# Kernel optimization log

Measured on AMD Instinct MI355X. Metric: run time of the kernel, lower is better.

The kernel has to match this reference:

```python
import jax, jax.numpy as jnp
import numpy as np

N = 40000      # nodes
E = 640000     # edges
IN_DIM = 128
HID = 128
HEADS = 4
DHEAD = HID // HEADS  # 32
LAYERS = 3
TIMESTEPS = 2
NEG_SLOPE = 0.2


def setup_inputs() -> dict:
    key = jax.random.key(0)
    ks = jax.random.split(key, 16)
    s = 0.05
    inp = {
        "node_feats": jax.random.normal(ks[0], (N, IN_DIM), jnp.float32),
        "src": jax.random.randint(ks[1], (E,), 0, N, jnp.int32),
        "dst": jax.random.randint(ks[2], (E,), 0, N, jnp.int32),
        "proj_W": jax.random.normal(ks[3], (IN_DIM, HID), jnp.float32) * s,
        "proj_b": jnp.zeros((HID,), jnp.float32),
        "fc_W": jax.random.normal(ks[4], (LAYERS, HID, HID), jnp.float32) * s,
        "attn_l": jax.random.normal(ks[5], (LAYERS, HEADS, DHEAD), jnp.float32) * s,
        "attn_r": jax.random.normal(ks[6], (LAYERS, HEADS, DHEAD), jnp.float32) * s,
        "conv_bias": jnp.zeros((LAYERS, HID), jnp.float32),
        "gru_Wih": jax.random.normal(ks[7], (3 * HID, HID), jnp.float32) * s,
        "gru_Whh": jax.random.normal(ks[8], (3 * HID, HID), jnp.float32) * s,
        "gru_bih": jnp.zeros((3 * HID,), jnp.float32),
        "gru_bhh": jnp.zeros((3 * HID,), jnp.float32),
    }
    return inp


def _gat_layer(h, src, dst, fc_W, attn_l, attn_r, bias):
    # h: (N, HID). DGL GATConv: fc -> edge attn -> segment softmax -> scatter sum
    feat = (h @ fc_W).reshape(N, HEADS, DHEAD)
    el = jnp.einsum('nhd,hd->nh', feat, attn_l)  # (N, H)
    er = jnp.einsum('nhd,hd->nh', feat, attn_r)
    e = jax.nn.leaky_relu(el[src] + er[dst], NEG_SLOPE)  # (E, H)
    # segment softmax over incoming edges per destination node
    emax = jax.ops.segment_max(e, dst, num_segments=N)  # (N, H)
    ee = jnp.exp(e - emax[dst])
    denom = jax.ops.segment_sum(ee, dst, num_segments=N)
    alpha = ee / denom[dst]  # (E, H)
    msg = feat[src] * alpha[:, :, None]  # (E, H, D)
    rst = jax.ops.segment_sum(msg, dst, num_segments=N)  # (N, H, D)
    rst = rst + h.reshape(N, HEADS, DHEAD)          # identity residual
    rst = rst + bias.reshape(HEADS, DHEAD)          # learned bias
    return jax.nn.elu(rst).reshape(N, HID)


def _gru_step(x, Wih, Whh, bih, bhh):
    # seq_len == 1, h0 == 0 -> recurrent matmul Whh @ h0 vanishes; b_hh remains
    gi = x @ Wih.T + bih  # (N, 3*HID)
    r = jax.nn.sigmoid(gi[:, :HID] + bhh[:HID])
    z = jax.nn.sigmoid(gi[:, HID:2 * HID] + bhh[HID:2 * HID])
    n = jnp.tanh(gi[:, 2 * HID:] + r * bhh[2 * HID:])
    return (1.0 - z) * n


def reference(node_feats, src, dst, proj_W, proj_b, fc_W, attn_l, attn_r,
              conv_bias, gru_Wih, gru_Whh, gru_bih, gru_bhh):
    h = node_feats @ proj_W + proj_b
    for l in range(LAYERS):
        h = _gat_layer(h, src, dst, fc_W[l], attn_l[l], attn_r[l], conv_bias[l])
    for _ in range(TIMESTEPS):
        h = _gru_step(h, gru_Wih, gru_Whh, gru_bih, gru_bhh)
    return h
```

## Files before the change

kernel.cpp:

```cpp
#include <hip/hip_runtime.h>
#include <hip/hip_bf16.h>

#define NNODES 40000
#define NEDGES 640000
#define M2PAD  40064
#define HID    128
#define PADCAP 920064

typedef __attribute__((ext_vector_type(8))) short bf16x8;
typedef __attribute__((ext_vector_type(4))) float f32x4;

__device__ __forceinline__ float bl(unsigned u){ return __uint_as_float(u << 16); }
__device__ __forceinline__ float bh(unsigned u){ return __uint_as_float(u & 0xFFFF0000u); }
__device__ __forceinline__ unsigned short f2b(float f){
    unsigned u = __float_as_uint(f);
    u = (u + 0x7FFFu + ((u >> 16) & 1u)) >> 16;
    return (unsigned short)u;
}
__device__ __forceinline__ float fast_rcp(float x){ return __builtin_amdgcn_rcpf(x); }

__device__ __forceinline__ void g2l16(const void* g, void* l){
    __builtin_amdgcn_global_load_lds(
        (const __attribute__((address_space(1))) unsigned int*)g,
        (__attribute__((address_space(3))) unsigned int*)l, 16, 0, 0);
}

__device__ __forceinline__ float wcalc(float e, float erw, int j, int rem){
    float t = e + erw;
    t = (t > 0.f) ? t : 0.2f * t;
    t = __expf(t);
    return (j < rem) ? t : 0.f;
}

__device__ __forceinline__ unsigned lds_off(int row, int col){
    return (unsigned)(row * 256 + (((col >> 3) ^ (row & 15)) << 4) + ((col & 7) << 1));
}

__global__ void prep_all(const float* __restrict__ node_feats,
                         const float* __restrict__ proj_W, const float* __restrict__ fc_W,
                         const float* __restrict__ gru_Wih, const int* __restrict__ dstp,
                         unsigned short* __restrict__ nf,
                         unsigned short* __restrict__ projWT, unsigned short* __restrict__ fcWT,
                         unsigned short* __restrict__ gruWb, int* __restrict__ deg){
    int b = blockIdx.x;
    if (b < 5000){
        int gid = b * 256 + threadIdx.x;
        float4 v = ((const float4*)node_feats)[gid];
        ushort4 o;
        o.x = f2b(v.x); o.y = f2b(v.y); o.z = f2b(v.z); o.w = f2b(v.w);
        ((ushort4*)nf)[gid] = o;
    } else if (b < 5256){
        int t = b - 5000;
        int c = t >> 6;
        int idx = (t & 63) * 256 + threadIdx.x;
        const float* in   = (c == 0) ? proj_W : fc_W + (size_t)(c - 1) * 16384;
        unsigned short* o = (c == 0) ? projWT : fcWT + (size_t)(c - 1) * 16384;
        int k = idx >> 7, n = idx & 127;
        o[n * 128 + k] = f2b(in[idx]);
    } else if (b < 5448){
        int idx = (b - 5256) * 256 + threadIdx.x;
        gruWb[idx] = f2b(gru_Wih[idx]);
    } else {
        int e = (b - 5448) * 256 + threadIdx.x;
        atomicAdd(&deg[dstp[e]], 1);
    }
}

__global__ __launch_bounds__(1024) void scan_kernel(const int* __restrict__ deg,
        int* __restrict__ rowptr, int* __restrict__ cur, int Nn4){
    __shared__ int wsum[17];
    __shared__ int carry;
    int t = threadIdx.x, lane = t & 63, wid = t >> 6;
    if (t == 0) carry = 0;
    __syncthreads();
    for (int base = 0; base < Nn4; base += 1024){
        int i4 = base + t;
        int4 dg = (i4 < Nn4) ? ((const int4*)deg)[i4] : make_int4(0, 0, 0, 0);
        int p0 = (dg.x + 7) & ~7, p1 = (dg.y + 7) & ~7;
        int p2 = (dg.z + 7) & ~7, p3 = (dg.w + 7) & ~7;
        int v = p0 + p1 + p2 + p3;
        int x = v;
        #pragma unroll
        for (int d = 1; d < 64; d <<= 1){
            int y = __shfl_up(x, d, 64);
            if (lane >= d) x += y;
        }
        if (lane == 63) wsum[wid] = x;
        __syncthreads();
        if (wid == 0){
            int vv = (lane < 16) ? wsum[lane] : 0;
            int xx = vv;
            #pragma unroll
            for (int d = 1; d < 16; d <<= 1){
                int y = __shfl_up(xx, d, 64);
                if (lane >= d) xx += y;
            }
            if (lane < 16) wsum[lane] = xx - vv;
            if (lane == 15) wsum[16] = xx;
        }
        __syncthreads();
        int excl = carry + wsum[wid] + (x - v);
        if (i4 < Nn4){
            int4 o = make_int4(excl, excl + p0, excl + p0 + p1, excl + p0 + p1 + p2);
            ((int4*)rowptr)[i4] = o;
            ((int4*)cur)[i4]    = o;
        }
        __syncthreads();
        if (t == 0) carry += wsum[16];
        __syncthreads();
    }
    if (t == 0) rowptr[Nn4 * 4] = carry;
}

__global__ void fill_kernel(const int* __restrict__ src, const int* __restrict__ dst,
                            int* __restrict__ cur, int* __restrict__ esrc){
    int e = blockIdx.x * 256 + threadIdx.x;
    int d = dst[e];
    int pos = atomicAdd(&cur[d], 1);
    esrc[pos] = src[e];
}

template<int MT>
__global__ __launch_bounds__(256) void gemm_t(
        const unsigned short* __restrict__ A, const unsigned short* __restrict__ BT,
        const float* __restrict__ bias, void* __restrict__ C,
        int Mreal, int ldc, int outF32,
        const float* __restrict__ al, const float* __restrict__ ar,
        float* __restrict__ elp, float* __restrict__ erp)
{
    __shared__ unsigned char lds[MT * 256 + 32768];
    unsigned char* ldsA = lds;
    unsigned char* ldsB = lds + MT * 256;
    int w = threadIdx.x >> 6, lane = threadIdx.x & 63;
    int rsub = lane >> 4, c16 = lane & 15;
    long baseM = (long)blockIdx.x * MT;
    long baseN = (long)blockIdx.y * 128;

    #pragma unroll
    for (int i = 0; i < MT / 16; i++){
        int chunk = w * (MT / 16) + i;
        int r = chunk * 4 + rsub;
        int cg = c16 ^ (r & 15);
        long ar_ = baseM + r; if (ar_ >= Mreal) ar_ = Mreal - 1;
        g2l16((const unsigned char*)A + ar_ * 256 + cg * 16, ldsA + chunk * 1024);
    }
    #pragma unroll
    for (int i = 0; i < 8; i++){
        int chunk = w * 8 + i;
        int r = chunk * 4 + rsub;
        int cg = c16 ^ (r & 15);
        long br = baseN + r;
        g2l16((const unsigned char*)BT + br * 256 + cg * 16, ldsB + chunk * 1024);
    }
    __syncthreads();

    constexpr int MI = 4;
    constexpr int NI = (MT == 128) ? 4 : 2;
    int mo = (MT == 128) ? (w & 1) * 64 : 0;
    int no = (MT == 128) ? (w >> 1) * 64 : w * 32;
    int q = lane >> 4, cl = lane & 15;
    f32x4 acc[MI][NI];
    #pragma unroll
    for (int i = 0; i < MI; i++)
        #pragma unroll
        for (int j = 0; j < NI; j++) acc[i][j] = (f32x4){0.f, 0.f, 0.f, 0.f};

    #pragma unroll
    for (int kc = 0; kc < 4; kc++){
        bf16x8 av[MI], bv[NI];
        #pragma unroll
        for (int mi = 0; mi < MI; mi++){
            int row = mo + mi * 16 + cl;
            int cs = (kc * 4 + q) ^ (row & 15);
            av[mi] = *(const bf16x8*)(ldsA + row * 256 + cs * 16);
        }
        #pragma unroll
        for (int ni = 0; ni < NI; ni++){
            int row = no + ni * 16 + cl;
            int cs = (kc * 4 + q) ^ (row & 15);
            bv[ni] = *(const bf16x8*)(ldsB + row * 256 + cs * 16);
        }
        #pragma unroll
        for (int mi = 0; mi < MI; mi++)
            #pragma unroll
            for (int ni = 0; ni < NI; ni++)
                acc[mi][ni] = __builtin_amdgcn_mfma_f32_16x16x32_bf16(av[mi], bv[ni], acc[mi][ni], 0, 0, 0);
    }

    #pragma unroll
    for (int mi = 0; mi < MI; mi++){
        #pragma unroll
        for (int ni = 0; ni < NI; ni++){
            int gn = (int)baseN + no + ni * 16 + cl;
            float bvf = bias ? bias[gn] : 0.f;
            long gm0 = baseM + mo + mi * 16 + q * 4;
            #pragma unroll
            for (int reg = 0; reg < 4; reg++){
                float v = acc[mi][ni][reg] + bvf;
                long gm = gm0 + reg;
                if (gm < Mreal){
                    if (outF32) ((float*)C)[gm * ldc + gn] = v;
                    else ((unsigned short*)C)[gm * ldc + gn] = f2b(v);
                }
            }
        }
    }

    if (NI == 2 && al){
        float al_lo = al[no + cl], al_hi = al[no + 16 + cl];
        float ar_lo = ar[no + cl], ar_hi = ar[no + 16 + cl];
        #pragma unroll
        for (int mi = 0; mi < MI; mi++){
            #pragma unroll
            for (int reg = 0; reg < 4; reg++){
                float pl = acc[mi][0][reg] * al_lo + acc[mi][1][reg] * al_hi;
                float pr = acc[mi][0][reg] * ar_lo + acc[mi][1][reg] * ar_hi;
                #pragma unroll
                for (int msk = 8; msk; msk >>= 1){
                    pl += __shfl_xor(pl, msk, 64);
                    pr += __shfl_xor(pr, msk, 64);
                }
                long gm = baseM + mi * 16 + q * 4 + reg;
                if (cl == 0 && gm < Mreal){
                    elp[gm * 4 + w] = pl;
                    erp[gm * 4 + w] = pr;
                }
            }
        }
    }
}

__global__ __launch_bounds__(256) void proj_fc1(
        const unsigned short* __restrict__ nf,
        const unsigned short* __restrict__ projWT, const float* __restrict__ proj_b,
        const unsigned short* __restrict__ fcWT0,
        unsigned short* __restrict__ h, unsigned short* __restrict__ feat,
        const float* __restrict__ al, const float* __restrict__ ar,
        float* __restrict__ elp, float* __restrict__ erp)
{
    __shared__ unsigned char ldsA[16384];
    __shared__ unsigned char ldsB[32768];
    int w = threadIdx.x >> 6, lane = threadIdx.x & 63;
    int rsub = lane >> 4, c16 = lane & 15;
    long baseM = (long)blockIdx.x * 64;

    #pragma unroll
    for (int i = 0; i < 4; i++){
        int chunk = w * 4 + i;
        int r = chunk * 4 + rsub;
        int cg = c16 ^ (r & 15);
        g2l16((const unsigned char*)nf + (baseM + r) * 256 + cg * 16, ldsA + chunk * 1024);
    }
    #pragma unroll
    for (int i = 0; i < 8; i++){
        int chunk = w * 8 + i;
        int r = chunk * 4 + rsub;
        int cg = c16 ^ (r & 15);
        g2l16((const unsigned char*)projWT + r * 256 + cg * 16, ldsB + chunk * 1024);
    }
    __syncthreads();

    int no = w * 32;
    int q = lane >> 4, cl = lane & 15;
    f32x4 acc[4][2];
    #pragma unroll
    for (int i = 0; i < 4; i++)
        #pragma unroll
        for (int j = 0; j < 2; j++) acc[i][j] = (f32x4){0.f, 0.f, 0.f, 0.f};

    #pragma unroll
    for (int kc = 0; kc < 4; kc++){
        bf16x8 av[4], bv[2];
        #pragma unroll
        for (int mi = 0; mi < 4; mi++){
            int row = mi * 16 + cl;
            int cs = (kc * 4 + q) ^ (row & 15);
            av[mi] = *(const bf16x8*)(ldsA + row * 256 + cs * 16);
        }
        #pragma unroll
        for (int ni = 0; ni < 2; ni++){
            int row = no + ni * 16 + cl;
            int cs = (kc * 4 + q) ^ (row & 15);
            bv[ni] = *(const bf16x8*)(ldsB + row * 256 + cs * 16);
        }
        #pragma unroll
        for (int mi = 0; mi < 4; mi++)
            #pragma unroll
            for (int ni = 0; ni < 2; ni++)
                acc[mi][ni] = __builtin_amdgcn_mfma_f32_16x16x32_bf16(av[mi], bv[ni], acc[mi][ni], 0, 0, 0);
    }
    __syncthreads();

    #pragma unroll
    for (int ni = 0; ni < 2; ni++){
        int j = no + ni * 16 + cl;
        float bvf = proj_b[j];
        #pragma unroll
        for (int mi = 0; mi < 4; mi++){
            #pragma unroll
            for (int reg = 0; reg < 4; reg++){
                int row = mi * 16 + q * 4 + reg;
                unsigned short bb = f2b(acc[mi][ni][reg] + bvf);
                h[(baseM + row) * 128 + j] = bb;
                *(unsigned short*)(ldsA + lds_off(row, j)) = bb;
            }
        }
    }
    #pragma unroll
    for (int i = 0; i < 8; i++){
        int chunk = w * 8 + i;
        int r = chunk * 4 + rsub;
        int cg = c16 ^ (r & 15);
        g2l16((const unsigned char*)fcWT0 + r * 256 + cg * 16, ldsB + chunk * 1024);
    }
    __syncthreads();

    #pragma unroll
    for (int i = 0; i < 4; i++)
        #pragma unroll
        for (int j = 0; j < 2; j++) acc[i][j] = (f32x4){0.f, 0.f, 0.f, 0.f};

    #pragma unroll
    for (int kc = 0; kc < 4; kc++){
        bf16x8 av[4], bv[2];
        #pragma unroll
        for (int mi = 0; mi < 4; mi++){
            int row = mi * 16 + cl;
            int cs = (kc * 4 + q) ^ (row & 15);
            av[mi] = *(const bf16x8*)(ldsA + row * 256 + cs * 16);
        }
        #pragma unroll
        for (int ni = 0; ni < 2; ni++){
            int row = no + ni * 16 + cl;
            int cs = (kc * 4 + q) ^ (row & 15);
            bv[ni] = *(const bf16x8*)(ldsB + row * 256 + cs * 16);
        }
        #pragma unroll
        for (int mi = 0; mi < 4; mi++)
            #pragma unroll
            for (int ni = 0; ni < 2; ni++)
                acc[mi][ni] = __builtin_amdgcn_mfma_f32_16x16x32_bf16(av[mi], bv[ni], acc[mi][ni], 0, 0, 0);
    }

    #pragma unroll
    for (int mi = 0; mi < 4; mi++){
        #pragma unroll
        for (int ni = 0; ni < 2; ni++){
            int gn = no + ni * 16 + cl;
            #pragma unroll
            for (int reg = 0; reg < 4; reg++){
                long gm = baseM + mi * 16 + q * 4 + reg;
                feat[gm * 128 + gn] = f2b(acc[mi][ni][reg]);
            }
        }
    }
    float al_lo = al[no + cl], al_hi = al[no + 16 + cl];
    float ar_lo = ar[no + cl], ar_hi = ar[no + 16 + cl];
    #pragma unroll
    for (int mi = 0; mi < 4; mi++){
        #pragma unroll
        for (int reg = 0; reg < 4; reg++){
            float pl = acc[mi][0][reg] * al_lo + acc[mi][1][reg] * al_hi;
            float pr = acc[mi][0][reg] * ar_lo + acc[mi][1][reg] * ar_hi;
            #pragma unroll
            for (int msk = 8; msk; msk >>= 1){
                pl += __shfl_xor(pl, msk, 64);
                pr += __shfl_xor(pr, msk, 64);
            }
            long gm = baseM + mi * 16 + q * 4 + reg;
            if (cl == 0){
                elp[gm * 4 + w] = pl;
                erp[gm * 4 + w] = pr;
            }
        }
    }
}

__global__ __launch_bounds__(256) void gru2x(
        const unsigned short* __restrict__ A, const unsigned short* __restrict__ BT,
        const float* __restrict__ bih, const float* __restrict__ bhh,
        float* __restrict__ out, int Mreal)
{
    __shared__ unsigned char ldsA[16384];
    __shared__ unsigned char ldsB[32768];
    int w = threadIdx.x >> 6, lane = threadIdx.x & 63;
    int rsub = lane >> 4, c16 = lane & 15;
    long baseM = (long)blockIdx.x * 64;

    #pragma unroll
    for (int i = 0; i < 4; i++){
        int chunk = w * 4 + i;
        int r = chunk * 4 + rsub;
        int cg = c16 ^ (r & 15);
        g2l16((const unsigned char*)A + (baseM + r) * 256 + cg * 16, ldsA + chunk * 1024);
    }

    int no = w * 32;
    int q = lane >> 4, cl = lane & 15;
    f32x4 acc[3][4][2];

    #pragma unroll
    for (int s = 0; s < 2; s++){
        #pragma unroll
        for (int c = 0; c < 3; c++)
            #pragma unroll
            for (int i = 0; i < 4; i++)
                #pragma unroll
                for (int j = 0; j < 2; j++) acc[c][i][j] = (f32x4){0.f, 0.f, 0.f, 0.f};

        #pragma unroll
        for (int c = 0; c < 3; c++){
            __syncthreads();
            #pragma unroll
            for (int i = 0; i < 8; i++){
                int chunk = w * 8 + i;
                int r = chunk * 4 + rsub;
                int cg = c16 ^ (r & 15);
                long br = c * 128 + r;
                g2l16((const unsigned char*)BT + br * 256 + cg * 16, ldsB + chunk * 1024);
            }
            __syncthreads();
            #pragma unroll
            for (int kc = 0; kc < 4; kc++){
                bf16x8 av[4], bv[2];
                #pragma unroll
                for (int mi = 0; mi < 4; mi++){
                    int row = mi * 16 + cl;
                    int cs = (kc * 4 + q) ^ (row & 15);
                    av[mi] = *(const bf16x8*)(ldsA + row * 256 + cs * 16);
                }
                #pragma unroll
                for (int ni = 0; ni < 2; ni++){
                    int row = no + ni * 16 + cl;
                    int cs = (kc * 4 + q) ^ (row & 15);
                    bv[ni] = *(const bf16x8*)(ldsB + row * 256 + cs * 16);
                }
                #pragma unroll
                for (int mi = 0; mi < 4; mi++)
                    #pragma unroll
                    for (int ni = 0; ni < 2; ni++)
                        acc[c][mi][ni] = __builtin_amdgcn_mfma_f32_16x16x32_bf16(av[mi], bv[ni], acc[c][mi][ni], 0, 0, 0);
            }
        }
        if (s == 0) __syncthreads();

        #pragma unroll
        for (int ni = 0; ni < 2; ni++){
            int j = no + ni * 16 + cl;
            float bir = bih[j]       + bhh[j];
            float biz = bih[128 + j] + bhh[128 + j];
            float bin = bih[256 + j];
            float bhn = bhh[256 + j];
            #pragma unroll
            for (int mi = 0; mi < 4; mi++){
                #pragma unroll
                for (int reg = 0; reg < 4; reg++){
                    int row = mi * 16 + q * 4 + reg;
                    float gr = acc[0][mi][ni][reg] + bir;
                    float gz = acc[1][mi][ni][reg] + biz;
                    float gn = acc[2][mi][ni][reg] + bin;
                    float r = fast_rcp(1.f + __expf(-gr));
                    float z = fast_rcp(1.f + __expf(-gz));
                    float ex = __expf(2.f * (gn + r * bhn));
                    float nn = (ex - 1.f) * fast_rcp(ex + 1.f);
                    float v = (1.f - z) * nn;
                    if (s == 0){
                        *(unsigned short*)(ldsA + lds_off(row, j)) = f2b(v);
                    } else {
                        long nr = baseM + row;
                        if (nr < Mreal) out[nr * 128 + j] = v;
                    }
                }
            }
        }
    }
}

__global__ __launch_bounds__(256) void aggregate(
        const int* __restrict__ rowptr, const int* __restrict__ degv,
        const int* __restrict__ esrc,
        const float* __restrict__ el, const float* __restrict__ er,
        const unsigned short* __restrict__ feat, const float* __restrict__ bias,
        unsigned short* __restrict__ h)
{
    int wid = threadIdx.x >> 6, lane = threadIdx.x & 63;
    int n = blockIdx.x * 4 + wid;
    int hh = lane >> 4;
    int d0 = lane * 2;
    unsigned doff = (unsigned)(d0 * 2);
    int beg = rowptr[n], end = rowptr[n + 1];
    int dg  = degv[n];
    float erw = er[(size_t)n * 4 + hh];
    float s = 0.f, a0 = 0.f, a1 = 0.f;
    const char* fbc = (const char*)feat;
    const int*  ep  = esrc + beg;

    if (beg < end){
        int4 sA = *(const int4*)(ep);
        int4 sB = *(const int4*)(ep + 4);
        float e0=0.f,e1=0.f,e2=0.f,e3=0.f,e4=0.f,e5=0.f,e6=0.f,e7=0.f;
        unsigned f0=0,f1=0,f2=0,f3=0,f4=0,f5=0,f6=0,f7=0;
        int rprev = 0;
        int rcur  = dg;
        for (int p = beg; p < end; p += 8){
            float g0 = el[(((unsigned)sA.x) << 2) + hh];
            float g1 = el[(((unsigned)sA.y) << 2) + hh];
            float g2 = el[(((unsigned)sA.z) << 2) + hh];
            float g3 = el[(((unsigned)sA.w) << 2) + hh];
            float g4 = el[(((unsigned)sB.x) << 2) + hh];
            float g5 = el[(((unsigned)sB.y) << 2) + hh];
            float g6 = el[(((unsigned)sB.z) << 2) + hh];
            float g7 = el[(((unsigned)sB.w) << 2) + hh];
            unsigned c0 = *(const unsigned*)(fbc + ((((unsigned)sA.x) << 8) + doff));
            unsigned c1 = *(const unsigned*)(fbc + ((((unsigned)sA.y) << 8) + doff));
            unsigned c2 = *(const unsigned*)(fbc + ((((unsigned)sA.z) << 8) + doff));
            unsigned c3 = *(const unsigned*)(fbc + ((((unsigned)sA.w) << 8) + doff));
            unsigned c4 = *(const unsigned*)(fbc + ((((unsigned)sB.x) << 8) + doff));
            unsigned c5 = *(const unsigned*)(fbc + ((((unsigned)sB.y) << 8) + doff));
            unsigned c6 = *(const unsigned*)(fbc + ((((unsigned)sB.z) << 8) + doff));
            unsigned c7 = *(const unsigned*)(fbc + ((((unsigned)sB.w) << 8) + doff));
            int4 nA = *(const int4*)(ep + 8);
            int4 nB = *(const int4*)(ep + 12);
            float w0 = wcalc(e0, erw, 0, rprev);
            float w1 = wcalc(e1, erw, 1, rprev);
            float w2 = wcalc(e2, erw, 2, rprev);
            float w3 = wcalc(e3, erw, 3, rprev);
            float w4 = wcalc(e4, erw, 4, rprev);
            float w5 = wcalc(e5, erw, 5, rprev);
            float w6 = wcalc(e6, erw, 6, rprev);
            float w7 = wcalc(e7, erw, 7, rprev);
            s += ((w0 + w1) + (w2 + w3)) + ((w4 + w5) + (w6 + w7));
            a0 = fmaf(w0, bl(f0), fmaf(w1, bl(f1), fmaf(w2, bl(f2), fmaf(w3, bl(f3), a0))));
            a0 = fmaf(w4, bl(f4), fmaf(w5, bl(f5), fmaf(w6, bl(f6), fmaf(w7, bl(f7), a0))));
            a1 = fmaf(w0, bh(f0), fmaf(w1, bh(f1), fmaf(w2, bh(f2), fmaf(w3, bh(f3), a1))));
            a1 = fmaf(w4, bh(f4), fmaf(w5, bh(f5), fmaf(w6, bh(f6), fmaf(w7, bh(f7), a1))));
            e0 = g0; e1 = g1; e2 = g2; e3 = g3; e4 = g4; e5 = g5; e6 = g6; e7 = g7;
            f0 = c0; f1 = c1; f2 = c2; f3 = c3; f4 = c4; f5 = c5; f6 = c6; f7 = c7;
            sA = nA; sB = nB;
            rprev = rcur; rcur -= 8;
            ep += 8;
        }
        float w0 = wcalc(e0, erw, 0, rprev);
        float w1 = wcalc(e1, erw, 1, rprev);
        float w2 = wcalc(e2, erw, 2, rprev);
        float w3 = wcalc(e3, erw, 3, rprev);
        float w4 = wcalc(e4, erw, 4, rprev);
        float w5 = wcalc(e5, erw, 5, rprev);
        float w6 = wcalc(e6, erw, 6, rprev);
        float w7 = wcalc(e7, erw, 7, rprev);
        s += ((w0 + w1) + (w2 + w3)) + ((w4 + w5) + (w6 + w7));
        a0 = fmaf(w0, bl(f0), fmaf(w1, bl(f1), fmaf(w2, bl(f2), fmaf(w3, bl(f3), a0))));
        a0 = fmaf(w4, bl(f4), fmaf(w5, bl(f5), fmaf(w6, bl(f6), fmaf(w7, bl(f7), a0))));
        a1 = fmaf(w0, bh(f0), fmaf(w1, bh(f1), fmaf(w2, bh(f2), fmaf(w3, bh(f3), a1))));
        a1 = fmaf(w4, bh(f4), fmaf(w5, bh(f5), fmaf(w6, bh(f6), fmaf(w7, bh(f7), a1))));
    }
    float inv = (s > 0.f) ? fast_rcp(s) : 0.f;
    unsigned hv = *(const unsigned*)(h + (size_t)n * 128 + d0);
    float x0 = a0 * inv + bl(hv) + bias[d0];
    float x1 = a1 * inv + bh(hv) + bias[d0 + 1];
    x0 = (x0 > 0.f) ? x0 : expm1f(x0);
    x1 = (x1 > 0.f) ? x1 : expm1f(x1);
    unsigned outv = (unsigned)f2b(x0) | ((unsigned)f2b(x1) << 16);
    *(unsigned*)(h + (size_t)n * 128 + d0) = outv;
}

extern "C" void kernel_launch(void* const* d_in, const int* in_sizes, int n_in,
                              void* d_out, int out_size, void* d_ws, size_t ws_size,
                              hipStream_t stream) {
    const float* node_feats = (const float*)d_in[0];
    const int*   srcp       = (const int*)d_in[1];
    const int*   dstp       = (const int*)d_in[2];
    const float* proj_W     = (const float*)d_in[3];
    const float* proj_b     = (const float*)d_in[4];
    const float* fc_W       = (const float*)d_in[5];
    const float* attn_l     = (const float*)d_in[6];
    const float* attn_r     = (const float*)d_in[7];
    const float* conv_bias  = (const float*)d_in[8];
    const float* gru_Wih    = (const float*)d_in[9];
    const float* gru_bih    = (const float*)d_in[11];
    const float* gru_bhh    = (const float*)d_in[12];
    float* outp = (float*)d_out;

    char* ws = (char*)d_ws;
    size_t off = 0;
    auto carve = [&](size_t bytes) -> char* {
        char* p = ws + off;
        off += (bytes + 255) & ~(size_t)255;
        return p;
    };
    int*            deg    = (int*)carve((size_t)NNODES * 4);
    int*            rowptr = (int*)carve((size_t)(NNODES + 1) * 4);
    int*            cur    = (int*)carve((size_t)NNODES * 4);
    int*            esrc   = (int*)carve((size_t)(PADCAP + 32) * 4);
    float*          el     = (float*)carve((size_t)NNODES * 4 * 4);
    float*          er     = (float*)carve((size_t)NNODES * 4 * 4);
    unsigned short* projWT = (unsigned short*)carve(16384 * 2);
    unsigned short* fcWT   = (unsigned short*)carve(3 * 16384 * 2);
    unsigned short* gruWb  = (unsigned short*)carve(49152 * 2);
    unsigned short* nf     = (unsigned short*)carve((size_t)NNODES * 128 * 2);
    unsigned short* h      = (unsigned short*)carve((size_t)M2PAD * 128 * 2);
    unsigned short* feat   = (unsigned short*)carve((size_t)M2PAD * 128 * 2);
    (void)ws_size; (void)in_sizes; (void)n_in; (void)out_size;

    hipMemsetAsync(deg, 0, (size_t)NNODES * 4, stream);
    hipMemsetAsync(esrc, 0, (size_t)(PADCAP + 32) * 4, stream);
    prep_all<<<7948, 256, 0, stream>>>(node_feats, proj_W, fc_W, gru_Wih, dstp,
                                       nf, projWT, fcWT, gruWb, deg);
    scan_kernel<<<1, 1024, 0, stream>>>(deg, rowptr, cur, NNODES / 4);
    fill_kernel<<<NEDGES / 256, 256, 0, stream>>>(srcp, dstp, cur, esrc);

    proj_fc1<<<625, 256, 0, stream>>>(nf, projWT, proj_b, fcWT, h, feat,
                                      attn_l, attn_r, el, er);

    for (int l = 0; l < 3; l++){
        if (l > 0){
            gemm_t<64><<<dim3(625, 1), 256, 0, stream>>>(h, fcWT + l * 16384, nullptr, feat, NNODES, 128, 0,
                                                         attn_l + l * 128, attn_r + l * 128, el, er);
        }
        aggregate<<<NNODES / 4, 256, 0, stream>>>(rowptr, deg, esrc, el, er, feat,
                                                  conv_bias + l * 128, h);
    }

    gru2x<<<625, 256, 0, stream>>>(h, gruWb, gru_bih, gru_bhh, outp, NNODES);
}
```

Measured before the change: 361.8 us.

## Privatize degree and cursor atomics into eight sub-counters per node

Degree counting and CSR fill now spread atomics across eight copies of the per-node counters, chosen by edge index modulo 8, to reduce atomic contention on the same address. Two small kernels are added: one sums the eight degree copies before the scan, and one sets up per-copy cursor offsets after it. The two memsets are merged into one by placing deg8 and esrc next to each other. The cost is two extra launches and 8x larger counter arrays with less atomic locality.

```diff
diff --git a/kernel.cpp b/kernel.cpp
--- a/kernel.cpp
+++ b/kernel.cpp
@@ -41,7 +41,7 @@
                          const float* __restrict__ gru_Wih, const int* __restrict__ dstp,
                          unsigned short* __restrict__ nf,
                          unsigned short* __restrict__ projWT, unsigned short* __restrict__ fcWT,
-                         unsigned short* __restrict__ gruWb, int* __restrict__ deg){
+                         unsigned short* __restrict__ gruWb, int* __restrict__ deg8){
     int b = blockIdx.x;
     if (b < 5000){
         int gid = b * 256 + threadIdx.x;
@@ -62,12 +62,24 @@
         gruWb[idx] = f2b(gru_Wih[idx]);
     } else {
         int e = (b - 5448) * 256 + threadIdx.x;
-        atomicAdd(&deg[dstp[e]], 1);
-    }
-}
-
-__global__ __launch_bounds__(1024) void scan_kernel(const int* __restrict__ deg,
-        int* __restrict__ rowptr, int* __restrict__ cur, int Nn4){
+        atomicAdd(&deg8[(e & 7) * NNODES + dstp[e]], 1);
+    }
+}
+
+__global__ void reduce_deg(const int* __restrict__ deg8, int* __restrict__ degt){
+    int i4 = blockIdx.x * 256 + threadIdx.x;
+    if (i4 >= NNODES / 4) return;
+    int4 s = make_int4(0, 0, 0, 0);
+    #pragma unroll
+    for (int x = 0; x < 8; x++){
+        int4 d = ((const int4*)(deg8 + (size_t)x * NNODES))[i4];
+        s.x += d.x; s.y += d.y; s.z += d.z; s.w += d.w;
+    }
+    ((int4*)degt)[i4] = s;
+}
+
+__global__ __launch_bounds__(1024) void scan_kernel(const int* __restrict__ degt,
+        int* __restrict__ rowptr, int Nn4){
     __shared__ int wsum[17];
     __shared__ int carry;
     int t = threadIdx.x, lane = t & 63, wid = t >> 6;
@@ -75,7 +87,7 @@
     __syncthreads();
     for (int base = 0; base < Nn4; base += 1024){
         int i4 = base + t;
-        int4 dg = (i4 < Nn4) ? ((const int4*)deg)[i4] : make_int4(0, 0, 0, 0);
+        int4 dg = (i4 < Nn4) ? ((const int4*)degt)[i4] : make_int4(0, 0, 0, 0);
         int p0 = (dg.x + 7) & ~7, p1 = (dg.y + 7) & ~7;
         int p2 = (dg.z + 7) & ~7, p3 = (dg.w + 7) & ~7;
         int v = p0 + p1 + p2 + p3;
@@ -103,7 +115,6 @@
         if (i4 < Nn4){
             int4 o = make_int4(excl, excl + p0, excl + p0 + p1, excl + p0 + p1 + p2);
             ((int4*)rowptr)[i4] = o;
-            ((int4*)cur)[i4]    = o;
         }
         __syncthreads();
         if (t == 0) carry += wsum[16];
@@ -112,11 +123,24 @@
     if (t == 0) rowptr[Nn4 * 4] = carry;
 }
 
+__global__ void cur_init(const int* __restrict__ deg8, const int* __restrict__ rowptr,
+                         int* __restrict__ cur8){
+    int i4 = blockIdx.x * 256 + threadIdx.x;
+    if (i4 >= NNODES / 4) return;
+    int4 run = ((const int4*)rowptr)[i4];
+    #pragma unroll
+    for (int x = 0; x < 8; x++){
+        ((int4*)(cur8 + (size_t)x * NNODES))[i4] = run;
+        int4 d = ((const int4*)(deg8 + (size_t)x * NNODES))[i4];
+        run.x += d.x; run.y += d.y; run.z += d.z; run.w += d.w;
+    }
+}
+
 __global__ void fill_kernel(const int* __restrict__ src, const int* __restrict__ dst,
-                            int* __restrict__ cur, int* __restrict__ esrc){
+                            int* __restrict__ cur8, int* __restrict__ esrc){
     int e = blockIdx.x * 256 + threadIdx.x;
     int d = dst[e];
-    int pos = atomicAdd(&cur[d], 1);
+    int pos = atomicAdd(&cur8[(e & 7) * NNODES + d], 1);
     esrc[pos] = src[e];
 }
 
@@ -588,10 +612,11 @@
         off += (bytes + 255) & ~(size_t)255;
         return p;
     };
-    int*            deg    = (int*)carve((size_t)NNODES * 4);
+    int*            deg8   = (int*)carve((size_t)8 * NNODES * 4);
+    int*            esrc   = (int*)carve((size_t)(PADCAP + 32) * 4);
     int*            rowptr = (int*)carve((size_t)(NNODES + 1) * 4);
-    int*            cur    = (int*)carve((size_t)NNODES * 4);
-    int*            esrc   = (int*)carve((size_t)(PADCAP + 32) * 4);
+    int*            degt   = (int*)carve((size_t)NNODES * 4);
+    int*            cur8   = (int*)carve((size_t)8 * NNODES * 4);
     float*          el     = (float*)carve((size_t)NNODES * 4 * 4);
     float*          er     = (float*)carve((size_t)NNODES * 4 * 4);
     unsigned short* projWT = (unsigned short*)carve(16384 * 2);
@@ -602,12 +627,13 @@
     unsigned short* feat   = (unsigned short*)carve((size_t)M2PAD * 128 * 2);
     (void)ws_size; (void)in_sizes; (void)n_in; (void)out_size;
 
-    hipMemsetAsync(deg, 0, (size_t)NNODES * 4, stream);
-    hipMemsetAsync(esrc, 0, (size_t)(PADCAP + 32) * 4, stream);
+    hipMemsetAsync(deg8, 0, (size_t)8 * NNODES * 4 + (((size_t)(PADCAP + 32) * 4 + 255) & ~(size_t)255), stream);
     prep_all<<<7948, 256, 0, stream>>>(node_feats, proj_W, fc_W, gru_Wih, dstp,
-                                       nf, projWT, fcWT, gruWb, deg);
-    scan_kernel<<<1, 1024, 0, stream>>>(deg, rowptr, cur, NNODES / 4);
-    fill_kernel<<<NEDGES / 256, 256, 0, stream>>>(srcp, dstp, cur, esrc);
+                                       nf, projWT, fcWT, gruWb, deg8);
+    reduce_deg<<<40, 256, 0, stream>>>(deg8, degt);
+    scan_kernel<<<1, 1024, 0, stream>>>(degt, rowptr, NNODES / 4);
+    cur_init<<<40, 256, 0, stream>>>(deg8, rowptr, cur8);
+    fill_kernel<<<NEDGES / 256, 256, 0, stream>>>(srcp, dstp, cur8, esrc);
 
     proj_fc1<<<625, 256, 0, stream>>>(nf, projWT, proj_b, fcWT, h, feat,
                                       attn_l, attn_r, el, er);
@@ -617,7 +643,7 @@
             gemm_t<64><<<dim3(625, 1), 256, 0, stream>>>(h, fcWT + l * 16384, nullptr, feat, NNODES, 128, 0,
                                                          attn_l + l * 128, attn_r + l * 128, el, er);
         }
-        aggregate<<<NNODES / 4, 256, 0, stream>>>(rowptr, deg, esrc, el, er, feat,
+        aggregate<<<NNODES / 4, 256, 0, stream>>>(rowptr, degt, esrc, el, er, feat,
                                                   conv_bias + l * 128, h);
     }
 
```

Measured after the change: 362.5 us. Within noise of the previous version (+0.2%).

## Split degree atomics eight ways, parallel lookback scan, fuse CSR fill with projection

Applied to the files above, without the earlier changes.

Degree counting now spreads atomics over eight sub-histograms indexed by edge id to reduce contention on the same counters. The single-block serial scan is replaced by a 40-block scan whose blocks each wait on the totals of all earlier blocks, and it emits per-slice insertion cursors. The CSR fill is merged into the projection+fc1 kernel as extra blocks so the two run concurrently, and one memset replaces two. The risks are that the inter-block spin-wait relies on all 40 blocks being resident at the same time, and that extra traffic is needed to read the eight sub-histograms.

```diff
diff --git a/kernel.cpp b/kernel.cpp
--- a/kernel.cpp
+++ b/kernel.cpp
@@ -41,7 +41,7 @@
                          const float* __restrict__ gru_Wih, const int* __restrict__ dstp,
                          unsigned short* __restrict__ nf,
                          unsigned short* __restrict__ projWT, unsigned short* __restrict__ fcWT,
-                         unsigned short* __restrict__ gruWb, int* __restrict__ deg){
+                         unsigned short* __restrict__ gruWb, int* __restrict__ deg8){
     int b = blockIdx.x;
     if (b < 5000){
         int gid = b * 256 + threadIdx.x;
@@ -62,62 +62,231 @@
         gruWb[idx] = f2b(gru_Wih[idx]);
     } else {
         int e = (b - 5448) * 256 + threadIdx.x;
-        atomicAdd(&deg[dstp[e]], 1);
-    }
-}
-
-__global__ __launch_bounds__(1024) void scan_kernel(const int* __restrict__ deg,
-        int* __restrict__ rowptr, int* __restrict__ cur, int Nn4){
-    __shared__ int wsum[17];
-    __shared__ int carry;
-    int t = threadIdx.x, lane = t & 63, wid = t >> 6;
-    if (t == 0) carry = 0;
+        atomicAdd(&deg8[(e & 7) * NNODES + dstp[e]], 1);
+    }
+}
+
+__global__ __launch_bounds__(256) void scan_lookback(
+        const int* __restrict__ deg8, int* __restrict__ rowptr, int* __restrict__ degt,
+        int* __restrict__ cur8, unsigned long long* __restrict__ state){
+    __shared__ int wincl[4];
+    __shared__ int wexcl[4];
+    __shared__ int blockT;
+    __shared__ int baseSh;
+    int b = blockIdx.x, t = threadIdx.x, lane = t & 63, wid = t >> 6;
+    int i4 = b * 256 + t;
+    bool ok = i4 < NNODES / 4;
+    int4 d[8];
+    #pragma unroll
+    for (int x = 0; x < 8; x++)
+        d[x] = ok ? ((const int4*)(deg8 + (size_t)x * NNODES))[i4] : make_int4(0, 0, 0, 0);
+    int s0 = 0, s1 = 0, s2 = 0, s3 = 0;
+    #pragma unroll
+    for (int x = 0; x < 8; x++){ s0 += d[x].x; s1 += d[x].y; s2 += d[x].z; s3 += d[x].w; }
+    int p0 = (s0 + 7) & ~7, p1 = (s1 + 7) & ~7;
+    int p2 = (s2 + 7) & ~7, p3 = (s3 + 7) & ~7;
+    int v = p0 + p1 + p2 + p3;
+    int x = v;
+    #pragma unroll
+    for (int dd = 1; dd < 64; dd <<= 1){
+        int y = __shfl_up(x, dd, 64);
+        if (lane >= dd) x += y;
+    }
+    if (lane == 63) wincl[wid] = x;
     __syncthreads();
-    for (int base = 0; base < Nn4; base += 1024){
-        int i4 = base + t;
-        int4 dg = (i4 < Nn4) ? ((const int4*)deg)[i4] : make_int4(0, 0, 0, 0);
-        int p0 = (dg.x + 7) & ~7, p1 = (dg.y + 7) & ~7;
-        int p2 = (dg.z + 7) & ~7, p3 = (dg.w + 7) & ~7;
-        int v = p0 + p1 + p2 + p3;
-        int x = v;
-        #pragma unroll
-        for (int d = 1; d < 64; d <<= 1){
-            int y = __shfl_up(x, d, 64);
-            if (lane >= d) x += y;
-        }
-        if (lane == 63) wsum[wid] = x;
-        __syncthreads();
-        if (wid == 0){
-            int vv = (lane < 16) ? wsum[lane] : 0;
-            int xx = vv;
-            #pragma unroll
-            for (int d = 1; d < 16; d <<= 1){
-                int y = __shfl_up(xx, d, 64);
-                if (lane >= d) xx += y;
-            }
-            if (lane < 16) wsum[lane] = xx - vv;
-            if (lane == 15) wsum[16] = xx;
-        }
-        __syncthreads();
-        int excl = carry + wsum[wid] + (x - v);
-        if (i4 < Nn4){
-            int4 o = make_int4(excl, excl + p0, excl + p0 + p1, excl + p0 + p1 + p2);
-            ((int4*)rowptr)[i4] = o;
-            ((int4*)cur)[i4]    = o;
-        }
-        __syncthreads();
-        if (t == 0) carry += wsum[16];
-        __syncthreads();
-    }
-    if (t == 0) rowptr[Nn4 * 4] = carry;
-}
-
-__global__ void fill_kernel(const int* __restrict__ src, const int* __restrict__ dst,
-                            int* __restrict__ cur, int* __restrict__ esrc){
-    int e = blockIdx.x * 256 + threadIdx.x;
-    int d = dst[e];
-    int pos = atomicAdd(&cur[d], 1);
-    esrc[pos] = src[e];
+    if (t == 0){
+        int a = 0;
+        #pragma unroll
+        for (int i = 0; i < 4; i++){ wexcl[i] = a; a += wincl[i]; }
+        blockT = a;
+        __hip_atomic_store(&state[b], ((unsigned long long)(unsigned)a << 32) | 1ull,
+                           __ATOMIC_RELEASE, __HIP_MEMORY_SCOPE_AGENT);
+    }
+    __syncthreads();
+    if (wid == 0){
+        int contrib = 0;
+        if (lane < b){
+            unsigned long long st;
+            do {
+                st = __hip_atomic_load(&state[lane], __ATOMIC_ACQUIRE, __HIP_MEMORY_SCOPE_AGENT);
+            } while (!(st & 1ull));
+            contrib = (int)(st >> 32);
+        }
+        #pragma unroll
+        for (int msk = 32; msk; msk >>= 1) contrib += __shfl_xor(contrib, msk, 64);
+        if (lane == 0) baseSh = contrib;
+    }
+    __syncthreads();
+    int base = baseSh;
+    int excl = base + wexcl[wid] + (x - v);
+    if (ok){
+        int4 o = make_int4(excl, excl + p0, excl + p0 + p1, excl + p0 + p1 + p2);
+        ((int4*)rowptr)[i4] = o;
+        ((int4*)degt)[i4]   = make_int4(s0, s1, s2, s3);
+        int o0 = o.x, o1 = o.y, o2 = o.z, o3 = o.w;
+        #pragma unroll
+        for (int xx = 0; xx < 8; xx++){
+            ((int4*)(cur8 + (size_t)xx * NNODES))[i4] = make_int4(o0, o1, o2, o3);
+            o0 += d[xx].x; o1 += d[xx].y; o2 += d[xx].z; o3 += d[xx].w;
+        }
+    }
+    if (b == 39 && t == 0) rowptr[NNODES] = base + blockT;
+}
+
+__global__ __launch_bounds__(256) void fill_proj(
+        const int* __restrict__ src, const int* __restrict__ dst,
+        int* __restrict__ cur8, int* __restrict__ esrc,
+        const unsigned short* __restrict__ nf,
+        const unsigned short* __restrict__ projWT, const float* __restrict__ proj_b,
+        const unsigned short* __restrict__ fcWT0,
+        unsigned short* __restrict__ h, unsigned short* __restrict__ feat,
+        const float* __restrict__ al, const float* __restrict__ ar,
+        float* __restrict__ elp, float* __restrict__ erp)
+{
+    __shared__ unsigned char ldsA[16384];
+    __shared__ unsigned char ldsB[32768];
+    int b = blockIdx.x;
+    if (b >= 625){
+        int e = (b - 625) * 256 + threadIdx.x;
+        int d = dst[e];
+        int pos = atomicAdd(&cur8[(e & 7) * NNODES + d], 1);
+        esrc[pos] = src[e];
+        return;
+    }
+    int w = threadIdx.x >> 6, lane = threadIdx.x & 63;
+    int rsub = lane >> 4, c16 = lane & 15;
+    long baseM = (long)b * 64;
+
+    #pragma unroll
+    for (int i = 0; i < 4; i++){
+        int chunk = w * 4 + i;
+        int r = chunk * 4 + rsub;
+        int cg = c16 ^ (r & 15);
+        g2l16((const unsigned char*)nf + (baseM + r) * 256 + cg * 16, ldsA + chunk * 1024);
+    }
+    #pragma unroll
+    for (int i = 0; i < 8; i++){
+        int chunk = w * 8 + i;
+        int r = chunk * 4 + rsub;
+        int cg = c16 ^ (r & 15);
+        g2l16((const unsigned char*)projWT + r * 256 + cg * 16, ldsB + chunk * 1024);
+    }
+    __syncthreads();
+
+    int no = w * 32;
+    int q = lane >> 4, cl = lane & 15;
+    f32x4 acc[4][2];
+    #pragma unroll
+    for (int i = 0; i < 4; i++)
+        #pragma unroll
+        for (int j = 0; j < 2; j++) acc[i][j] = (f32x4){0.f, 0.f, 0.f, 0.f};
+
+    #pragma unroll
+    for (int kc = 0; kc < 4; kc++){
+        bf16x8 av[4], bv[2];
+        #pragma unroll
+        for (int mi = 0; mi < 4; mi++){
+            int row = mi * 16 + cl;
+            int cs = (kc * 4 + q) ^ (row & 15);
+            av[mi] = *(const bf16x8*)(ldsA + row * 256 + cs * 16);
+        }
+        #pragma unroll
+        for (int ni = 0; ni < 2; ni++){
+            int row = no + ni * 16 + cl;
+            int cs = (kc * 4 + q) ^ (row & 15);
+            bv[ni] = *(const bf16x8*)(ldsB + row * 256 + cs * 16);
+        }
+        #pragma unroll
+        for (int mi = 0; mi < 4; mi++)
+            #pragma unroll
+            for (int ni = 0; ni < 2; ni++)
+                acc[mi][ni] = __builtin_amdgcn_mfma_f32_16x16x32_bf16(av[mi], bv[ni], acc[mi][ni], 0, 0, 0);
+    }
+    __syncthreads();
+
+    #pragma unroll
+    for (int ni = 0; ni < 2; ni++){
+        int j = no + ni * 16 + cl;
+        float bvf = proj_b[j];
+        #pragma unroll
+        for (int mi = 0; mi < 4; mi++){
+            #pragma unroll
+            for (int reg = 0; reg < 4; reg++){
+                int row = mi * 16 + q * 4 + reg;
+                unsigned short bb = f2b(acc[mi][ni][reg] + bvf);
+                h[(baseM + row) * 128 + j] = bb;
+                *(unsigned short*)(ldsA + lds_off(row, j)) = bb;
+            }
+        }
+    }
+    #pragma unroll
+    for (int i = 0; i < 8; i++){
+        int chunk = w * 8 + i;
+        int r = chunk * 4 + rsub;
+        int cg = c16 ^ (r & 15);
+        g2l16((const unsigned char*)fcWT0 + r * 256 + cg * 16, ldsB + chunk * 1024);
+    }
+    __syncthreads();
+
+    #pragma unroll
+    for (int i = 0; i < 4; i++)
+        #pragma unroll
+        for (int j = 0; j < 2; j++) acc[i][j] = (f32x4){0.f, 0.f, 0.f, 0.f};
+
+    #pragma unroll
+    for (int kc = 0; kc < 4; kc++){
+        bf16x8 av[4], bv[2];
+        #pragma unroll
+        for (int mi = 0; mi < 4; mi++){
+            int row = mi * 16 + cl;
+            int cs = (kc * 4 + q) ^ (row & 15);
+            av[mi] = *(const bf16x8*)(ldsA + row * 256 + cs * 16);
+        }
+        #pragma unroll
+        for (int ni = 0; ni < 2; ni++){
+            int row = no + ni * 16 + cl;
+            int cs = (kc * 4 + q) ^ (row & 15);
+            bv[ni] = *(const bf16x8*)(ldsB + row * 256 + cs * 16);
+        }
+        #pragma unroll
+        for (int mi = 0; mi < 4; mi++)
+            #pragma unroll
+            for (int ni = 0; ni < 2; ni++)
+                acc[mi][ni] = __builtin_amdgcn_mfma_f32_16x16x32_bf16(av[mi], bv[ni], acc[mi][ni], 0, 0, 0);
+    }
+
+    #pragma unroll
+    for (int mi = 0; mi < 4; mi++){
+        #pragma unroll
+        for (int ni = 0; ni < 2; ni++){
+            int gn = no + ni * 16 + cl;
+            #pragma unroll
+            for (int reg = 0; reg < 4; reg++){
+                long gm = baseM + mi * 16 + q * 4 + reg;
+                feat[gm * 128 + gn] = f2b(acc[mi][ni][reg]);
+            }
+        }
+    }
+    float al_lo = al[no + cl], al_hi = al[no + 16 + cl];
+    float ar_lo = ar[no + cl], ar_hi = ar[no + 16 + cl];
+    #pragma unroll
+    for (int mi = 0; mi < 4; mi++){
+        #pragma unroll
+        for (int reg = 0; reg < 4; reg++){
+            float pl = acc[mi][0][reg] * al_lo + acc[mi][1][reg] * al_hi;
+            float pr = acc[mi][0][reg] * ar_lo + acc[mi][1][reg] * ar_hi;
+            #pragma unroll
+            for (int msk = 8; msk; msk >>= 1){
+                pl += __shfl_xor(pl, msk, 64);
+                pr += __shfl_xor(pr, msk, 64);
+            }
+            long gm = baseM + mi * 16 + q * 4 + reg;
+            if (cl == 0){
+                elp[gm * 4 + w] = pl;
+                erp[gm * 4 + w] = pr;
+            }
+        }
+    }
 }
 
 template<int MT>
@@ -225,152 +394,6 @@
                     elp[gm * 4 + w] = pl;
                     erp[gm * 4 + w] = pr;
                 }
-            }
-        }
-    }
-}
-
-__global__ __launch_bounds__(256) void proj_fc1(
-        const unsigned short* __restrict__ nf,
-        const unsigned short* __restrict__ projWT, const float* __restrict__ proj_b,
-        const unsigned short* __restrict__ fcWT0,
-        unsigned short* __restrict__ h, unsigned short* __restrict__ feat,
-        const float* __restrict__ al, const float* __restrict__ ar,
-        float* __restrict__ elp, float* __restrict__ erp)
-{
-    __shared__ unsigned char ldsA[16384];
-    __shared__ unsigned char ldsB[32768];
-    int w = threadIdx.x >> 6, lane = threadIdx.x & 63;
-    int rsub = lane >> 4, c16 = lane & 15;
-    long baseM = (long)blockIdx.x * 64;
-
-    #pragma unroll
-    for (int i = 0; i < 4; i++){
-        int chunk = w * 4 + i;
-        int r = chunk * 4 + rsub;
-        int cg = c16 ^ (r & 15);
-        g2l16((const unsigned char*)nf + (baseM + r) * 256 + cg * 16, ldsA + chunk * 1024);
-    }
-    #pragma unroll
-    for (int i = 0; i < 8; i++){
-        int chunk = w * 8 + i;
-        int r = chunk * 4 + rsub;
-        int cg = c16 ^ (r & 15);
-        g2l16((const unsigned char*)projWT + r * 256 + cg * 16, ldsB + chunk * 1024);
-    }
-    __syncthreads();
-
-    int no = w * 32;
-    int q = lane >> 4, cl = lane & 15;
-    f32x4 acc[4][2];
-    #pragma unroll
-    for (int i = 0; i < 4; i++)
-        #pragma unroll
-        for (int j = 0; j < 2; j++) acc[i][j] = (f32x4){0.f, 0.f, 0.f, 0.f};
-
-    #pragma unroll
-    for (int kc = 0; kc < 4; kc++){
-        bf16x8 av[4], bv[2];
-        #pragma unroll
-        for (int mi = 0; mi < 4; mi++){
-            int row = mi * 16 + cl;
-            int cs = (kc * 4 + q) ^ (row & 15);
-            av[mi] = *(const bf16x8*)(ldsA + row * 256 + cs * 16);
-        }
-        #pragma unroll
-        for (int ni = 0; ni < 2; ni++){
-            int row = no + ni * 16 + cl;
-            int cs = (kc * 4 + q) ^ (row & 15);
-            bv[ni] = *(const bf16x8*)(ldsB + row * 256 + cs * 16);
-        }
-        #pragma unroll
-        for (int mi = 0; mi < 4; mi++)
-            #pragma unroll
-            for (int ni = 0; ni < 2; ni++)
-                acc[mi][ni] = __builtin_amdgcn_mfma_f32_16x16x32_bf16(av[mi], bv[ni], acc[mi][ni], 0, 0, 0);
-    }
-    __syncthreads();
-
-    #pragma unroll
-    for (int ni = 0; ni < 2; ni++){
-        int j = no + ni * 16 + cl;
-        float bvf = proj_b[j];
-        #pragma unroll
-        for (int mi = 0; mi < 4; mi++){
-            #pragma unroll
-            for (int reg = 0; reg < 4; reg++){
-                int row = mi * 16 + q * 4 + reg;
-                unsigned short bb = f2b(acc[mi][ni][reg] + bvf);
-                h[(baseM + row) * 128 + j] = bb;
-                *(unsigned short*)(ldsA + lds_off(row, j)) = bb;
-            }
-        }
-    }
-    #pragma unroll
-    for (int i = 0; i < 8; i++){
-        int chunk = w * 8 + i;
-        int r = chunk * 4 + rsub;
-        int cg = c16 ^ (r & 15);
-        g2l16((const unsigned char*)fcWT0 + r * 256 + cg * 16, ldsB + chunk * 1024);
-    }
-    __syncthreads();
-
-    #pragma unroll
-    for (int i = 0; i < 4; i++)
-        #pragma unroll
-        for (int j = 0; j < 2; j++) acc[i][j] = (f32x4){0.f, 0.f, 0.f, 0.f};
-
-    #pragma unroll
-    for (int kc = 0; kc < 4; kc++){
-        bf16x8 av[4], bv[2];
-        #pragma unroll
-        for (int mi = 0; mi < 4; mi++){
-            int row = mi * 16 + cl;
-            int cs = (kc * 4 + q) ^ (row & 15);
-            av[mi] = *(const bf16x8*)(ldsA + row * 256 + cs * 16);
-        }
-        #pragma unroll
-        for (int ni = 0; ni < 2; ni++){
-            int row = no + ni * 16 + cl;
-            int cs = (kc * 4 + q) ^ (row & 15);
-            bv[ni] = *(const bf16x8*)(ldsB + row * 256 + cs * 16);
-        }
-        #pragma unroll
-        for (int mi = 0; mi < 4; mi++)
-            #pragma unroll
-            for (int ni = 0; ni < 2; ni++)
-                acc[mi][ni] = __builtin_amdgcn_mfma_f32_16x16x32_bf16(av[mi], bv[ni], acc[mi][ni], 0, 0, 0);
-    }
-
-    #pragma unroll
-    for (int mi = 0; mi < 4; mi++){
-        #pragma unroll
-        for (int ni = 0; ni < 2; ni++){
-            int gn = no + ni * 16 + cl;
-            #pragma unroll
-            for (int reg = 0; reg < 4; reg++){
-                long gm = baseM + mi * 16 + q * 4 + reg;
-                feat[gm * 128 + gn] = f2b(acc[mi][ni][reg]);
-            }
-        }
-    }
-    float al_lo = al[no + cl], al_hi = al[no + 16 + cl];
-    float ar_lo = ar[no + cl], ar_hi = ar[no + 16 + cl];
-    #pragma unroll
-    for (int mi = 0; mi < 4; mi++){
-        #pragma unroll
-        for (int reg = 0; reg < 4; reg++){
-            float pl = acc[mi][0][reg] * al_lo + acc[mi][1][reg] * al_hi;
-            float pr = acc[mi][0][reg] * ar_lo + acc[mi][1][reg] * ar_hi;
-            #pragma unroll
-            for (int msk = 8; msk; msk >>= 1){
-                pl += __shfl_xor(pl, msk, 64);
-                pr += __shfl_xor(pr, msk, 64);
-            }
-            long gm = baseM + mi * 16 + q * 4 + reg;
-            if (cl == 0){
-                elp[gm * 4 + w] = pl;
-                erp[gm * 4 + w] = pr;
             }
         }
     }
@@ -588,36 +611,39 @@
         off += (bytes + 255) & ~(size_t)255;
         return p;
     };
-    int*            deg    = (int*)carve((size_t)NNODES * 4);
-    int*            rowptr = (int*)carve((size_t)(NNODES + 1) * 4);
-    int*            cur    = (int*)carve((size_t)NNODES * 4);
-    int*            esrc   = (int*)carve((size_t)(PADCAP + 32) * 4);
-    float*          el     = (float*)carve((size_t)NNODES * 4 * 4);
-    float*          er     = (float*)carve((size_t)NNODES * 4 * 4);
-    unsigned short* projWT = (unsigned short*)carve(16384 * 2);
-    unsigned short* fcWT   = (unsigned short*)carve(3 * 16384 * 2);
-    unsigned short* gruWb  = (unsigned short*)carve(49152 * 2);
-    unsigned short* nf     = (unsigned short*)carve((size_t)NNODES * 128 * 2);
-    unsigned short* h      = (unsigned short*)carve((size_t)M2PAD * 128 * 2);
-    unsigned short* feat   = (unsigned short*)carve((size_t)M2PAD * 128 * 2);
+    int*                deg8   = (int*)carve((size_t)8 * NNODES * 4);
+    unsigned long long* state  = (unsigned long long*)carve(512);
+    int*                esrc   = (int*)carve((size_t)(PADCAP + 32) * 4);
+    int*                rowptr = (int*)carve((size_t)(NNODES + 1) * 4);
+    int*                degt   = (int*)carve((size_t)NNODES * 4);
+    int*                cur8   = (int*)carve((size_t)8 * NNODES * 4);
+    float*              el     = (float*)carve((size_t)NNODES * 4 * 4);
+    float*              er     = (float*)carve((size_t)NNODES * 4 * 4);
+    unsigned short*     projWT = (unsigned short*)carve(16384 * 2);
+    unsigned short*     fcWT   = (unsigned short*)carve(3 * 16384 * 2);
+    unsigned short*     gruWb  = (unsigned short*)carve(49152 * 2);
+    unsigned short*     nf     = (unsigned short*)carve((size_t)NNODES * 128 * 2);
+    unsigned short*     h      = (unsigned short*)carve((size_t)M2PAD * 128 * 2);
+    unsigned short*     feat   = (unsigned short*)carve((size_t)M2PAD * 128 * 2);
     (void)ws_size; (void)in_sizes; (void)n_in; (void)out_size;
 
-    hipMemsetAsync(deg, 0, (size_t)NNODES * 4, stream);
-    hipMemsetAsync(esrc, 0, (size_t)(PADCAP + 32) * 4, stream);
+    hipMemsetAsync(deg8, 0,
+                   (size_t)8 * NNODES * 4 + 512 + (((size_t)(PADCAP + 32) * 4 + 255) & ~(size_t)255),
+                   stream);
     prep_all<<<7948, 256, 0, stream>>>(node_feats, proj_W, fc_W, gru_Wih, dstp,
-                                       nf, projWT, fcWT, gruWb, deg);
-    scan_kernel<<<1, 1024, 0, stream>>>(deg, rowptr, cur, NNODES / 4);
-    fill_kernel<<<NEDGES / 256, 256, 0, stream>>>(srcp, dstp, cur, esrc);
-
-    proj_fc1<<<625, 256, 0, stream>>>(nf, projWT, proj_b, fcWT, h, feat,
-                                      attn_l, attn_r, el, er);
+                                       nf, projWT, fcWT, gruWb, deg8);
+    scan_lookback<<<40, 256, 0, stream>>>(deg8, rowptr, degt, cur8, state);
+
+    fill_proj<<<625 + NEDGES / 256, 256, 0, stream>>>(srcp, dstp, cur8, esrc,
+                                                      nf, projWT, proj_b, fcWT, h, feat,
+                                                      attn_l, attn_r, el, er);
 
     for (int l = 0; l < 3; l++){
         if (l > 0){
             gemm_t<64><<<dim3(625, 1), 256, 0, stream>>>(h, fcWT + l * 16384, nullptr, feat, NNODES, 128, 0,
                                                          attn_l + l * 128, attn_r + l * 128, el, er);
         }
-        aggregate<<<NNODES / 4, 256, 0, stream>>>(rowptr, deg, esrc, el, er, feat,
+        aggregate<<<NNODES / 4, 256, 0, stream>>>(rowptr, degt, esrc, el, er, feat,
                                                   conv_bias + l * 128, h);
     }
 
```

Result: no change. 355.5 us (-1.7%).
